# Kernel tuning notes

Hardware: AMD Instinct MI355X
Metric: run time of the kernel (lower is better)

The kernel has to match this reference:

```python
import jax, jax.numpy as jnp
import numpy as np

E = 96   # embed_dim; num_heads = 96 -> head_dim = 1, scale = 1.0
P = 4    # patch size (in_features 48 = 3 * 4 * 4)
NW = 4   # n_windows (hardcoded in apply_window_msa)


def setup_inputs() -> dict:
    key = jax.random.key(0)
    ks = jax.random.split(key, 5)
    x = jax.random.normal(ks[0], (16, 3, 256, 256), dtype=jnp.float32)
    lin_w = jax.random.normal(ks[1], (E, 48), dtype=jnp.float32) * (1.0 / np.sqrt(48).astype(np.float32))
    lin_b = jnp.zeros((E,), jnp.float32)
    in_proj_w = jax.random.normal(ks[2], (3 * E, E), dtype=jnp.float32) * (1.0 / np.sqrt(E).astype(np.float32))
    in_proj_b = jnp.zeros((3 * E,), jnp.float32)
    out_proj_w = jax.random.normal(ks[3], (E, E), dtype=jnp.float32) * (1.0 / np.sqrt(E).astype(np.float32))
    out_proj_b = jnp.zeros((E,), jnp.float32)
    return dict(x=x, lin_w=lin_w, lin_b=lin_b, in_proj_w=in_proj_w,
                in_proj_b=in_proj_b, out_proj_w=out_proj_w, out_proj_b=out_proj_b)


def reference(x, lin_w, lin_b, in_proj_w, in_proj_b, out_proj_w, out_proj_b):
    N, C, H, W = x.shape
    Hp, Wp = H // P, W // P
    # patch_merging: torch unfold(2,P,P).unfold(3,P,P) -> [N,C,Hp,Wp,P,P] -> reshape
    patches = x.reshape(N, C, Hp, P, Wp, P).transpose(0, 1, 2, 4, 3, 5)
    patches = patches.reshape(N, C * P * P, Hp, Wp)  # [N, 48, Hp, Wp]
    # apply_linear_on_axis(axis=1): acts as a 1x1 projection 48 -> E
    emb = jnp.einsum('nchw,ec->nehw', patches, lin_w) + lin_b[None, :, None, None]
    # apply_window_msa: raw reshape [N,E,Hp,Wp] -> [N, 4, L, E] (memory-order, faithful to source)
    wh, ww = Hp // 2, Wp // 2
    L = wh * ww
    xw = emb.reshape(N, NW, L, E).transpose(1, 0, 2, 3)  # [4, N, L, E]
    # torch MHA with batch_first=False: seq dim = N (samples), batch dim = L
    qkv = jnp.einsum('wnle,fe->wnlf', xw, in_proj_w) + in_proj_b  # [4, N, L, 3E]
    q, k, v = jnp.split(qkv, 3, axis=-1)  # each [4, N, L, E]; E heads of dim 1
    # head_dim = 1 -> scale = 1.0; scores over the N (sample) axis
    scores = jnp.einsum('wslh,wtlh->wlhst', q, k)        # [4, L, 96, N, N]
    attn = jax.nn.softmax(scores, axis=-1)
    out = jnp.einsum('wlhst,wtlh->wslh', attn, v)        # [4, N, L, E]
    out = jnp.einsum('wnle,fe->wnlf', out, out_proj_w) + out_proj_b
    hidden = out.transpose(1, 0, 2, 3).reshape(N, E, Hp, Wp)  # raw reshape, faithful
    return hidden
```

## Files before the change

### kernel.cpp

```cpp
#include <hip/hip_runtime.h>

#define EMB_STRIDE 393216

typedef __attribute__((ext_vector_type(8))) short short8;
typedef __attribute__((ext_vector_type(4))) float f32x4;
typedef __attribute__((ext_vector_type(2))) __fp16 f16x2;

#define MFMA16 __builtin_amdgcn_mfma_f32_16x16x32_bf16
#define SCHED_PIN() __builtin_amdgcn_sched_barrier(0)

static __device__ __forceinline__ short bf16h(float v) {
    unsigned u = __builtin_bit_cast(unsigned, v);
    unsigned r = (u + 0x7FFFu + ((u >> 16) & 1u)) >> 16;
    return (short)r;
}
static __device__ __forceinline__ float bf16f(short s) {
    unsigned u = ((unsigned)(unsigned short)s) << 16;
    return __builtin_bit_cast(float, u);
}
static __device__ __forceinline__ unsigned packsplit(float v) {
    const short h = bf16h(v);
    const float d = v - bf16f(h);
    const unsigned lo = __builtin_bit_cast(unsigned, d) >> 16;
    return ((unsigned)(unsigned short)h << 16) | lo;
}

__global__ __launch_bounds__(256) void k_prep(
    const float* __restrict__ lin_w, const float* __restrict__ in_w,
    const float* __restrict__ out_w,
    short* __restrict__ WH, short* __restrict__ WL2,
    short* __restrict__ WOH, short* __restrict__ WOL,
    short* __restrict__ WPH, short* __restrict__ WPL) {
    const int i0 = blockIdx.x * 256 + threadIdx.x;
    const int stride = gridDim.x * 256;
    for (int i = i0; i < 27648; i += stride) {
        int j = i & 7, g = (i >> 3) & 3, rest = i >> 5;
        int f = rest % 288, kc = rest / 288;
        float v = in_w[f * 96 + kc * 32 + g * 8 + j];
        short h = bf16h(v);
        WH[i] = h; WL2[i] = bf16h(v - bf16f(h));
    }
    for (int i = i0; i < 9216; i += stride) {
        int j = i & 7, g = (i >> 3) & 3, rest = i >> 5;
        int f = rest % 96, kc = rest / 96;
        float v = out_w[f * 96 + kc * 32 + g * 8 + j];
        short h = bf16h(v);
        WOH[i] = h; WOL[i] = bf16h(v - bf16f(h));
    }
    for (int i = i0; i < 6144; i += stride) {
        int j = i & 7, lane = (i >> 3) & 63, rest = i >> 9;
        int et = rest % 6, kc = rest / 6;
        int e = et * 16 + (lane & 15);
        int k = kc * 32 + (lane >> 4) * 8 + j;
        float v = (k < 48) ? lin_w[e * 48 + k] : 0.f;
        short h = bf16h(v);
        WPH[i] = h; WPL[i] = bf16h(v - bf16f(h));
    }
}

__global__ __launch_bounds__(256, 3) void k_patch(
    const float* __restrict__ x, const short* __restrict__ WPH,
    const short* __restrict__ WPL, const float* __restrict__ lin_b,
    unsigned* __restrict__ embp) {
    const int tid = threadIdx.x, wave = tid >> 6, lane = tid & 63;
    const int n = blockIdx.x >> 6;
    const int T = (blockIdx.x & 63) * 4 + wave;
    const int a = T >> 6, b = (T >> 2) & 15, cc = T & 3;
    const int col16 = lane & 15, grp = lane >> 4;
    const int d = col16 >> 2, g = col16 & 3;

    const int rowoff = (a * 4 + d) * 256 + b * 16 + cc * 4 + g;
    const int gA = (grp >> 1) * 65536 + (grp & 1) * 32768;
    const float* p0 = x + (size_t)n * 196608 + rowoff + gA;

    float v0[8], v1[8];
#pragma unroll
    for (int j = 0; j < 8; ++j) v0[j] = p0[j * 4096];
    if (grp < 2) {
#pragma unroll
        for (int j = 0; j < 8; ++j) v1[j] = p0[131072 - (grp >> 1) * 65536 + j * 4096];
    }
    SCHED_PIN();
    short8 Bh[2], Bl[2];
#pragma unroll
    for (int j = 0; j < 8; ++j) {
        const short h = bf16h(v0[j]);
        Bh[0][j] = h; Bl[0][j] = bf16h(v0[j] - bf16f(h));
        Bh[1][j] = 0; Bl[1][j] = 0;
    }
    if (grp < 2) {
#pragma unroll
        for (int j = 0; j < 8; ++j) {
            const short h = bf16h(v1[j]);
            Bh[1][j] = h; Bl[1][j] = bf16h(v1[j] - bf16f(h));
        }
    }

    f32x4 acc[6];
#pragma unroll
    for (int et = 0; et < 6; ++et) acc[et] = (f32x4){0.f, 0.f, 0.f, 0.f};
#pragma unroll
    for (int kc = 0; kc < 2; ++kc) {
        short8 AH[6], AL[6];
#pragma unroll
        for (int et = 0; et < 6; ++et)
            AH[et] = *(const short8*)(WPH + (kc * 6 + et) * 512 + lane * 8);
#pragma unroll
        for (int et = 0; et < 6; ++et)
            AL[et] = *(const short8*)(WPL + (kc * 6 + et) * 512 + lane * 8);
        SCHED_PIN();
#pragma unroll
        for (int et = 0; et < 6; ++et) acc[et] = MFMA16(AH[et], Bh[kc], acc[et], 0, 0, 0);
#pragma unroll
        for (int et = 0; et < 6; ++et) acc[et] = MFMA16(AH[et], Bl[kc], acc[et], 0, 0, 0);
#pragma unroll
        for (int et = 0; et < 6; ++et) acc[et] = MFMA16(AL[et], Bh[kc], acc[et], 0, 0, 0);
    }

    unsigned* ebase = embp + (size_t)n * EMB_STRIDE + T * 16 + col16;
#pragma unroll
    for (int et = 0; et < 6; ++et) {
        const float4 bv = *(const float4*)(lin_b + et * 16 + grp * 4);
        const float vr[4] = {acc[et][0] + bv.x, acc[et][1] + bv.y,
                             acc[et][2] + bv.z, acc[et][3] + bv.w};
#pragma unroll
        for (int r = 0; r < 4; ++r)
            ebase[(size_t)(et * 16 + grp * 4 + r) * 4096] = packsplit(vr[r]);
    }
}

__global__ __launch_bounds__(128, 3) void k_msa(
    const unsigned* __restrict__ embp,
    const short* __restrict__ WH, const short* __restrict__ WL2,
    const short* __restrict__ WOH, const short* __restrict__ WOL,
    const float* __restrict__ in_b, const float* __restrict__ out_b,
    float* __restrict__ out) {

    __shared__ unsigned AO[2][96 * 17];

    const int tid = threadIdx.x;
    const int half = tid >> 6, lane = tid & 63;
    const int wl0 = blockIdx.x * 2;
    const int n = lane & 15, g = lane >> 4;
    const int hoff = half * 1536;

    uint4 ub[12];
#pragma unroll
    for (int w = 0; w < 2; ++w) {
        const unsigned* xrow = embp + (size_t)n * EMB_STRIDE + (wl0 + w) * 96;
#pragma unroll
        for (int kc = 0; kc < 3; ++kc) {
            ub[(w * 3 + kc) * 2]     = *(const uint4*)(xrow + kc * 32 + g * 8);
            ub[(w * 3 + kc) * 2 + 1] = *(const uint4*)(xrow + kc * 32 + g * 8 + 4);
        }
    }
    SCHED_PIN();
    short8 Bh[2][3], Bl[2][3];
#pragma unroll
    for (int w = 0; w < 2; ++w)
#pragma unroll
        for (int kc = 0; kc < 3; ++kc) {
            const uint4 ua0 = ub[(w * 3 + kc) * 2], ua1 = ub[(w * 3 + kc) * 2 + 1];
            const unsigned ua[8] = {ua0.x, ua0.y, ua0.z, ua0.w, ua1.x, ua1.y, ua1.z, ua1.w};
#pragma unroll
            for (int j = 0; j < 8; ++j) {
                Bh[w][kc][j] = (short)(ua[j] >> 16);
                Bl[w][kc][j] = (short)(ua[j] & 0xffffu);
            }
        }

    f32x4 acc0[9], acc1[9];
#pragma unroll
    for (int a = 0; a < 9; ++a) {
        acc0[a] = (f32x4){0.f, 0.f, 0.f, 0.f};
        acc1[a] = (f32x4){0.f, 0.f, 0.f, 0.f};
    }
#pragma unroll
    for (int kc = 0; kc < 3; ++kc) {
        const short* whp = WH  + kc * 9216 + n * 32 + g * 8 + hoff;
        const short* wlp = WL2 + kc * 9216 + n * 32 + g * 8 + hoff;
#pragma unroll
        for (int t3 = 0; t3 < 3; ++t3) {
            short8 AH[3], AL[3];
#pragma unroll
            for (int i = 0; i < 3; ++i)
                AH[i] = *(const short8*)(whp + (t3 * 6 + i) * 512);
#pragma unroll
            for (int i = 0; i < 3; ++i)
                AL[i] = *(const short8*)(wlp + (t3 * 6 + i) * 512);
            SCHED_PIN();
#pragma unroll
            for (int i = 0; i < 3; ++i) {
                const int a = t3 * 3 + i;
                acc0[a] = MFMA16(AH[i], Bh[0][kc], acc0[a], 0, 0, 0);
                acc1[a] = MFMA16(AH[i], Bh[1][kc], acc1[a], 0, 0, 0);
                acc0[a] = MFMA16(AH[i], Bl[0][kc], acc0[a], 0, 0, 0);
                acc1[a] = MFMA16(AH[i], Bl[1][kc], acc1[a], 0, 0, 0);
                acc0[a] = MFMA16(AL[i], Bh[0][kc], acc0[a], 0, 0, 0);
                acc1[a] = MFMA16(AL[i], Bh[1][kc], acc1[a], 0, 0, 0);
            }
        }
    }
#pragma unroll
    for (int a = 0; a < 9; ++a) {
        const float4 bv = *(const float4*)(in_b + ((a / 3) * 6 + (a % 3)) * 16 + half * 48 + g * 4);
        acc0[a][0] += bv.x; acc0[a][1] += bv.y; acc0[a][2] += bv.z; acc0[a][3] += bv.w;
        acc1[a][0] += bv.x; acc1[a][1] += bv.y; acc1[a][2] += bv.z; acc1[a][3] += bv.w;
    }

    const int gbase = lane & 48;
#define ATT_BODY(ACC, W)                                                       \
    {                                                                          \
        const float q2 = ACC[c][r2] * 1.44269504f;                             \
        const f16x2 pk = __builtin_amdgcn_cvt_pkrtz(ACC[3 + c][r2], ACC[6 + c][r2]); \
        const int pki = __builtin_bit_cast(int, pk);                           \
        int kvr[16];                                                           \
        _Pragma("unroll")                                                      \
        for (int tt = 0; tt < 16; ++tt) kvr[tt] = __shfl(pki, gbase | tt, 64); \
        SCHED_PIN();                                                           \
        float sp[4] = {0.f, 0.f, 0.f, 0.f}, op[4] = {0.f, 0.f, 0.f, 0.f};      \
        _Pragma("unroll")                                                      \
        for (int tt = 0; tt < 16; ++tt) {                                      \
            const f16x2 kv2 = __builtin_bit_cast(f16x2, kvr[tt]);              \
            const float e = __builtin_amdgcn_exp2f(q2 * (float)kv2[0]);        \
            sp[tt & 3] += e;                                                   \
            op[tt & 3] = fmaf(e, (float)kv2[1], op[tt & 3]);                   \
        }                                                                      \
        const float s = (sp[0] + sp[1]) + (sp[2] + sp[3]);                     \
        const float o = (op[0] + op[1]) + (op[2] + op[3]);                     \
        AO[W][(half * 48 + c * 16 + g * 4 + r2) * 17 + n] =                    \
            packsplit(o * __builtin_amdgcn_rcpf(s));                           \
    }
#pragma unroll
    for (int c = 0; c < 3; ++c)
#pragma unroll
        for (int r2 = 0; r2 < 4; ++r2) {
            ATT_BODY(acc0, 0)
            ATT_BODY(acc1, 1)
        }
    __syncthreads();

    f32x4 oc0[3], oc1[3];
#pragma unroll
    for (int c2 = 0; c2 < 3; ++c2) {
        oc0[c2] = (f32x4){0.f, 0.f, 0.f, 0.f};
        oc1[c2] = (f32x4){0.f, 0.f, 0.f, 0.f};
    }
#pragma unroll
    for (int kc = 0; kc < 3; ++kc) {
        const short* whp = WOH + kc * 3072 + n * 32 + g * 8 + hoff;
        const short* wlp = WOL + kc * 3072 + n * 32 + g * 8 + hoff;
        short8 OAH[3], OAL[3];
#pragma unroll
        for (int c2 = 0; c2 < 3; ++c2) OAH[c2] = *(const short8*)(whp + c2 * 512);
#pragma unroll
        for (int c2 = 0; c2 < 3; ++c2) OAL[c2] = *(const short8*)(wlp + c2 * 512);
        unsigned u0[8], u1[8];
#pragma unroll
        for (int j = 0; j < 8; ++j) {
            u0[j] = AO[0][(kc * 32 + g * 8 + j) * 17 + n];
            u1[j] = AO[1][(kc * 32 + g * 8 + j) * 17 + n];
        }
        SCHED_PIN();
        short8 bh0, bl0, bh1, bl1;
#pragma unroll
        for (int j = 0; j < 8; ++j) {
            bh0[j] = (short)(u0[j] >> 16); bl0[j] = (short)(u0[j] & 0xffffu);
            bh1[j] = (short)(u1[j] >> 16); bl1[j] = (short)(u1[j] & 0xffffu);
        }
#pragma unroll
        for (int c2 = 0; c2 < 3; ++c2) oc0[c2] = MFMA16(OAH[c2], bh0, oc0[c2], 0, 0, 0);
#pragma unroll
        for (int c2 = 0; c2 < 3; ++c2) oc1[c2] = MFMA16(OAH[c2], bh1, oc1[c2], 0, 0, 0);
#pragma unroll
        for (int c2 = 0; c2 < 3; ++c2) oc0[c2] = MFMA16(OAH[c2], bl0, oc0[c2], 0, 0, 0);
#pragma unroll
        for (int c2 = 0; c2 < 3; ++c2) oc1[c2] = MFMA16(OAH[c2], bl1, oc1[c2], 0, 0, 0);
#pragma unroll
        for (int c2 = 0; c2 < 3; ++c2) oc0[c2] = MFMA16(OAL[c2], bh0, oc0[c2], 0, 0, 0);
#pragma unroll
        for (int c2 = 0; c2 < 3; ++c2) oc1[c2] = MFMA16(OAL[c2], bh1, oc1[c2], 0, 0, 0);
    }

#pragma unroll
    for (int c2 = 0; c2 < 3; ++c2) {
        const int fb = half * 48 + c2 * 16 + g * 4;
        const float4 ob = *(const float4*)(out_b + fb);
        const float4 vs0 = make_float4(oc0[c2][0] + ob.x, oc0[c2][1] + ob.y,
                                       oc0[c2][2] + ob.z, oc0[c2][3] + ob.w);
        const float4 vs1 = make_float4(oc1[c2][0] + ob.x, oc1[c2][1] + ob.y,
                                       oc1[c2][2] + ob.z, oc1[c2][3] + ob.w);
        *(float4*)(out + (size_t)n * EMB_STRIDE + wl0 * 96 + fb) = vs0;
        *(float4*)(out + (size_t)n * EMB_STRIDE + (wl0 + 1) * 96 + fb) = vs1;
    }
}

extern "C" void kernel_launch(void* const* d_in, const int* in_sizes, int n_in,
                              void* d_out, int out_size, void* d_ws, size_t ws_size,
                              hipStream_t stream) {
    const float* x     = (const float*)d_in[0];
    const float* lin_w = (const float*)d_in[1];
    const float* lin_b = (const float*)d_in[2];
    const float* in_w  = (const float*)d_in[3];
    const float* in_b  = (const float*)d_in[4];
    const float* out_w = (const float*)d_in[5];
    const float* out_b = (const float*)d_in[6];
    float* outp = (float*)d_out;

    unsigned* embp = (unsigned*)d_ws;
    short* WH  = (short*)((char*)d_ws + 25165824);
    short* WL2 = WH + 32768;
    short* WOH = WH + 65536;
    short* WOL = WH + 81920;
    short* WPH = WH + 98304;
    short* WPL = WH + 106496;

    k_prep<<<64, 256, 0, stream>>>(lin_w, in_w, out_w, WH, WL2, WOH, WOL, WPH, WPL);
    k_patch<<<1024, 256, 0, stream>>>(x, WPH, WPL, lin_b, embp);
    k_msa<<<2048, 128, 0, stream>>>(embp, WH, WL2, WOH, WOL, in_b, out_b, outp);
}
```

Before: 73.76 us.

## Split MSA work across six waves per block with shared-memory staging

The MSA kernel goes from 2 waves to 6 waves per block, so each wave owns 16 heads instead of 48. The input rows are staged once into shared memory rather than loaded by each wave, and K/V pairs are exchanged through shared memory instead of cross-lane shuffles. The aim is more parallelism and lower register pressure per wave, at the cost of extra LDS traffic and a block-wide barrier after the staging load.

```diff
diff --git a/kernel.cpp b/kernel.cpp
--- a/kernel.cpp
+++ b/kernel.cpp
@@ -129,137 +129,136 @@
     }
 }
 
-__global__ __launch_bounds__(128, 3) void k_msa(
+__global__ __launch_bounds__(384, 4) void k_msa(
     const unsigned* __restrict__ embp,
     const short* __restrict__ WH, const short* __restrict__ WL2,
     const short* __restrict__ WOH, const short* __restrict__ WOL,
     const float* __restrict__ in_b, const float* __restrict__ out_b,
     float* __restrict__ out) {
 
-    __shared__ unsigned AO[2][96 * 17];
+    __shared__ unsigned Xs[2 * 16 * 100];
+    __shared__ unsigned KV[2 * 96 * 20];
 
     const int tid = threadIdx.x;
-    const int half = tid >> 6, lane = tid & 63;
+    const int ht = tid >> 6, lane = tid & 63;
     const int wl0 = blockIdx.x * 2;
     const int n = lane & 15, g = lane >> 4;
-    const int hoff = half * 1536;
-
-    uint4 ub[12];
-#pragma unroll
-    for (int w = 0; w < 2; ++w) {
-        const unsigned* xrow = embp + (size_t)n * EMB_STRIDE + (wl0 + w) * 96;
-#pragma unroll
-        for (int kc = 0; kc < 3; ++kc) {
-            ub[(w * 3 + kc) * 2]     = *(const uint4*)(xrow + kc * 32 + g * 8);
-            ub[(w * 3 + kc) * 2 + 1] = *(const uint4*)(xrow + kc * 32 + g * 8 + 4);
-        }
-    }
-    SCHED_PIN();
-    short8 Bh[2][3], Bl[2][3];
-#pragma unroll
-    for (int w = 0; w < 2; ++w)
-#pragma unroll
-        for (int kc = 0; kc < 3; ++kc) {
-            const uint4 ua0 = ub[(w * 3 + kc) * 2], ua1 = ub[(w * 3 + kc) * 2 + 1];
-            const unsigned ua[8] = {ua0.x, ua0.y, ua0.z, ua0.w, ua1.x, ua1.y, ua1.z, ua1.w};
+
+    {
+        const int pos = tid * 4;
+        const int sn = pos / 96, se = pos % 96;
+#pragma unroll
+        for (int w = 0; w < 2; ++w) {
+            const uint4 v = *(const uint4*)(embp + (size_t)sn * EMB_STRIDE + (wl0 + w) * 96 + se);
+            *(uint4*)(&Xs[w * 1600 + sn * 100 + se]) = v;
+        }
+    }
+    __syncthreads();
+
+    f32x4 acc0[3], acc1[3];
+#pragma unroll
+    for (int i = 0; i < 3; ++i) {
+        acc0[i] = (f32x4){0.f, 0.f, 0.f, 0.f};
+        acc1[i] = (f32x4){0.f, 0.f, 0.f, 0.f};
+    }
+#pragma unroll
+    for (int kc = 0; kc < 3; ++kc) {
+        const uint4 xa0 = *(const uint4*)(&Xs[n * 100 + kc * 32 + g * 8]);
+        const uint4 xa1 = *(const uint4*)(&Xs[n * 100 + kc * 32 + g * 8 + 4]);
+        const uint4 xb0 = *(const uint4*)(&Xs[1600 + n * 100 + kc * 32 + g * 8]);
+        const uint4 xb1 = *(const uint4*)(&Xs[1600 + n * 100 + kc * 32 + g * 8 + 4]);
+        const short* whp = WH  + kc * 9216 + ht * 512 + n * 32 + g * 8;
+        const short* wlp = WL2 + kc * 9216 + ht * 512 + n * 32 + g * 8;
+        short8 AH[3], AL[3];
+#pragma unroll
+        for (int i = 0; i < 3; ++i) AH[i] = *(const short8*)(whp + i * 3072);
+#pragma unroll
+        for (int i = 0; i < 3; ++i) AL[i] = *(const short8*)(wlp + i * 3072);
+        SCHED_PIN();
+        short8 Bh0, Bl0, Bh1, Bl1;
+        {
+            const unsigned ua[8] = {xa0.x, xa0.y, xa0.z, xa0.w, xa1.x, xa1.y, xa1.z, xa1.w};
+            const unsigned ub[8] = {xb0.x, xb0.y, xb0.z, xb0.w, xb1.x, xb1.y, xb1.z, xb1.w};
 #pragma unroll
             for (int j = 0; j < 8; ++j) {
-                Bh[w][kc][j] = (short)(ua[j] >> 16);
-                Bl[w][kc][j] = (short)(ua[j] & 0xffffu);
+                Bh0[j] = (short)(ua[j] >> 16); Bl0[j] = (short)(ua[j] & 0xffffu);
+                Bh1[j] = (short)(ub[j] >> 16); Bl1[j] = (short)(ub[j] & 0xffffu);
             }
         }
-
-    f32x4 acc0[9], acc1[9];
-#pragma unroll
-    for (int a = 0; a < 9; ++a) {
-        acc0[a] = (f32x4){0.f, 0.f, 0.f, 0.f};
-        acc1[a] = (f32x4){0.f, 0.f, 0.f, 0.f};
-    }
-#pragma unroll
-    for (int kc = 0; kc < 3; ++kc) {
-        const short* whp = WH  + kc * 9216 + n * 32 + g * 8 + hoff;
-        const short* wlp = WL2 + kc * 9216 + n * 32 + g * 8 + hoff;
-#pragma unroll
-        for (int t3 = 0; t3 < 3; ++t3) {
-            short8 AH[3], AL[3];
-#pragma unroll
-            for (int i = 0; i < 3; ++i)
-                AH[i] = *(const short8*)(whp + (t3 * 6 + i) * 512);
-#pragma unroll
-            for (int i = 0; i < 3; ++i)
-                AL[i] = *(const short8*)(wlp + (t3 * 6 + i) * 512);
-            SCHED_PIN();
-#pragma unroll
-            for (int i = 0; i < 3; ++i) {
-                const int a = t3 * 3 + i;
-                acc0[a] = MFMA16(AH[i], Bh[0][kc], acc0[a], 0, 0, 0);
-                acc1[a] = MFMA16(AH[i], Bh[1][kc], acc1[a], 0, 0, 0);
-                acc0[a] = MFMA16(AH[i], Bl[0][kc], acc0[a], 0, 0, 0);
-                acc1[a] = MFMA16(AH[i], Bl[1][kc], acc1[a], 0, 0, 0);
-                acc0[a] = MFMA16(AL[i], Bh[0][kc], acc0[a], 0, 0, 0);
-                acc1[a] = MFMA16(AL[i], Bh[1][kc], acc1[a], 0, 0, 0);
-            }
-        }
-    }
-#pragma unroll
-    for (int a = 0; a < 9; ++a) {
-        const float4 bv = *(const float4*)(in_b + ((a / 3) * 6 + (a % 3)) * 16 + half * 48 + g * 4);
-        acc0[a][0] += bv.x; acc0[a][1] += bv.y; acc0[a][2] += bv.z; acc0[a][3] += bv.w;
-        acc1[a][0] += bv.x; acc1[a][1] += bv.y; acc1[a][2] += bv.z; acc1[a][3] += bv.w;
-    }
-
-    const int gbase = lane & 48;
-#define ATT_BODY(ACC, W)                                                       \
+#pragma unroll
+        for (int i = 0; i < 3; ++i) acc0[i] = MFMA16(AH[i], Bh0, acc0[i], 0, 0, 0);
+#pragma unroll
+        for (int i = 0; i < 3; ++i) acc1[i] = MFMA16(AH[i], Bh1, acc1[i], 0, 0, 0);
+#pragma unroll
+        for (int i = 0; i < 3; ++i) acc0[i] = MFMA16(AH[i], Bl0, acc0[i], 0, 0, 0);
+#pragma unroll
+        for (int i = 0; i < 3; ++i) acc1[i] = MFMA16(AH[i], Bl1, acc1[i], 0, 0, 0);
+#pragma unroll
+        for (int i = 0; i < 3; ++i) acc0[i] = MFMA16(AL[i], Bh0, acc0[i], 0, 0, 0);
+#pragma unroll
+        for (int i = 0; i < 3; ++i) acc1[i] = MFMA16(AL[i], Bh1, acc1[i], 0, 0, 0);
+    }
+#pragma unroll
+    for (int i = 0; i < 3; ++i) {
+        const float4 bv = *(const float4*)(in_b + i * 96 + ht * 16 + g * 4);
+        acc0[i][0] += bv.x; acc0[i][1] += bv.y; acc0[i][2] += bv.z; acc0[i][3] += bv.w;
+        acc1[i][0] += bv.x; acc1[i][1] += bv.y; acc1[i][2] += bv.z; acc1[i][3] += bv.w;
+    }
+
+#pragma unroll
+    for (int r2 = 0; r2 < 4; ++r2) {
+        const int h = ht * 16 + g * 4 + r2;
+        const f16x2 p0 = __builtin_amdgcn_cvt_pkrtz(acc0[1][r2], acc0[2][r2]);
+        const f16x2 p1 = __builtin_amdgcn_cvt_pkrtz(acc1[1][r2], acc1[2][r2]);
+        KV[h * 20 + n] = __builtin_bit_cast(unsigned, p0);
+        KV[1920 + h * 20 + n] = __builtin_bit_cast(unsigned, p1);
+    }
+
+    unsigned ao0[4], ao1[4];
+#define ATT_BODY(ACC, WOFF, AOARR)                                             \
     {                                                                          \
-        const float q2 = ACC[c][r2] * 1.44269504f;                             \
-        const f16x2 pk = __builtin_amdgcn_cvt_pkrtz(ACC[3 + c][r2], ACC[6 + c][r2]); \
-        const int pki = __builtin_bit_cast(int, pk);                           \
-        int kvr[16];                                                           \
-        _Pragma("unroll")                                                      \
-        for (int tt = 0; tt < 16; ++tt) kvr[tt] = __shfl(pki, gbase | tt, 64); \
-        SCHED_PIN();                                                           \
+        const float q2 = ACC[0][r2] * 1.44269504f;                             \
+        const uint4* row = (const uint4*)(&KV[WOFF + (ht * 16 + g * 4 + r2) * 20]); \
+        const uint4 ra = row[0], rb = row[1], rc = row[2], rd = row[3];        \
+        const unsigned kv[16] = {ra.x, ra.y, ra.z, ra.w, rb.x, rb.y, rb.z, rb.w, \
+                                 rc.x, rc.y, rc.z, rc.w, rd.x, rd.y, rd.z, rd.w}; \
         float sp[4] = {0.f, 0.f, 0.f, 0.f}, op[4] = {0.f, 0.f, 0.f, 0.f};      \
         _Pragma("unroll")                                                      \
         for (int tt = 0; tt < 16; ++tt) {                                      \
-            const f16x2 kv2 = __builtin_bit_cast(f16x2, kvr[tt]);              \
+            const f16x2 kv2 = __builtin_bit_cast(f16x2, kv[tt]);               \
             const float e = __builtin_amdgcn_exp2f(q2 * (float)kv2[0]);        \
             sp[tt & 3] += e;                                                   \
             op[tt & 3] = fmaf(e, (float)kv2[1], op[tt & 3]);                   \
         }                                                                      \
         const float s = (sp[0] + sp[1]) + (sp[2] + sp[3]);                     \
         const float o = (op[0] + op[1]) + (op[2] + op[3]);                     \
-        AO[W][(half * 48 + c * 16 + g * 4 + r2) * 17 + n] =                    \
-            packsplit(o * __builtin_amdgcn_rcpf(s));                           \
-    }
-#pragma unroll
-    for (int c = 0; c < 3; ++c)
-#pragma unroll
-        for (int r2 = 0; r2 < 4; ++r2) {
-            ATT_BODY(acc0, 0)
-            ATT_BODY(acc1, 1)
-        }
+        AOARR[r2] = packsplit(o * __builtin_amdgcn_rcpf(s));                   \
+    }
+#pragma unroll
+    for (int r2 = 0; r2 < 4; ++r2) {
+        ATT_BODY(acc0, 0, ao0)
+        ATT_BODY(acc1, 1920, ao1)
+    }
+
+#pragma unroll
+    for (int r2 = 0; r2 < 4; ++r2) {
+        const int h = ht * 16 + g * 4 + r2;
+        KV[h * 20 + n] = ao0[r2];
+        KV[1920 + h * 20 + n] = ao1[r2];
+    }
     __syncthreads();
 
-    f32x4 oc0[3], oc1[3];
-#pragma unroll
-    for (int c2 = 0; c2 < 3; ++c2) {
-        oc0[c2] = (f32x4){0.f, 0.f, 0.f, 0.f};
-        oc1[c2] = (f32x4){0.f, 0.f, 0.f, 0.f};
-    }
+    f32x4 oc0 = (f32x4){0.f, 0.f, 0.f, 0.f};
+    f32x4 oc1 = (f32x4){0.f, 0.f, 0.f, 0.f};
 #pragma unroll
     for (int kc = 0; kc < 3; ++kc) {
-        const short* whp = WOH + kc * 3072 + n * 32 + g * 8 + hoff;
-        const short* wlp = WOL + kc * 3072 + n * 32 + g * 8 + hoff;
-        short8 OAH[3], OAL[3];
-#pragma unroll
-        for (int c2 = 0; c2 < 3; ++c2) OAH[c2] = *(const short8*)(whp + c2 * 512);
-#pragma unroll
-        for (int c2 = 0; c2 < 3; ++c2) OAL[c2] = *(const short8*)(wlp + c2 * 512);
+        const short8 OAH = *(const short8*)(WOH + kc * 3072 + ht * 512 + n * 32 + g * 8);
+        const short8 OAL = *(const short8*)(WOL + kc * 3072 + ht * 512 + n * 32 + g * 8);
         unsigned u0[8], u1[8];
 #pragma unroll
         for (int j = 0; j < 8; ++j) {
-            u0[j] = AO[0][(kc * 32 + g * 8 + j) * 17 + n];
-            u1[j] = AO[1][(kc * 32 + g * 8 + j) * 17 + n];
+            u0[j] = KV[(kc * 32 + g * 8 + j) * 20 + n];
+            u1[j] = KV[1920 + (kc * 32 + g * 8 + j) * 20 + n];
         }
         SCHED_PIN();
         short8 bh0, bl0, bh1, bl1;
@@ -268,28 +267,21 @@
             bh0[j] = (short)(u0[j] >> 16); bl0[j] = (short)(u0[j] & 0xffffu);
             bh1[j] = (short)(u1[j] >> 16); bl1[j] = (short)(u1[j] & 0xffffu);
         }
-#pragma unroll
-        for (int c2 = 0; c2 < 3; ++c2) oc0[c2] = MFMA16(OAH[c2], bh0, oc0[c2], 0, 0, 0);
-#pragma unroll
-        for (int c2 = 0; c2 < 3; ++c2) oc1[c2] = MFMA16(OAH[c2], bh1, oc1[c2], 0, 0, 0);
-#pragma unroll
-        for (int c2 = 0; c2 < 3; ++c2) oc0[c2] = MFMA16(OAH[c2], bl0, oc0[c2], 0, 0, 0);
-#pragma unroll
-        for (int c2 = 0; c2 < 3; ++c2) oc1[c2] = MFMA16(OAH[c2], bl1, oc1[c2], 0, 0, 0);
-#pragma unroll
-        for (int c2 = 0; c2 < 3; ++c2) oc0[c2] = MFMA16(OAL[c2], bh0, oc0[c2], 0, 0, 0);
-#pragma unroll
-        for (int c2 = 0; c2 < 3; ++c2) oc1[c2] = MFMA16(OAL[c2], bh1, oc1[c2], 0, 0, 0);
-    }
-
-#pragma unroll
-    for (int c2 = 0; c2 < 3; ++c2) {
-        const int fb = half * 48 + c2 * 16 + g * 4;
+        oc0 = MFMA16(OAH, bh0, oc0, 0, 0, 0);
+        oc1 = MFMA16(OAH, bh1, oc1, 0, 0, 0);
+        oc0 = MFMA16(OAH, bl0, oc0, 0, 0, 0);
+        oc1 = MFMA16(OAH, bl1, oc1, 0, 0, 0);
+        oc0 = MFMA16(OAL, bh0, oc0, 0, 0, 0);
+        oc1 = MFMA16(OAL, bh1, oc1, 0, 0, 0);
+    }
+
+    {
+        const int fb = ht * 16 + g * 4;
         const float4 ob = *(const float4*)(out_b + fb);
-        const float4 vs0 = make_float4(oc0[c2][0] + ob.x, oc0[c2][1] + ob.y,
-                                       oc0[c2][2] + ob.z, oc0[c2][3] + ob.w);
-        const float4 vs1 = make_float4(oc1[c2][0] + ob.x, oc1[c2][1] + ob.y,
-                                       oc1[c2][2] + ob.z, oc1[c2][3] + ob.w);
+        const float4 vs0 = make_float4(oc0[0] + ob.x, oc0[1] + ob.y,
+                                       oc0[2] + ob.z, oc0[3] + ob.w);
+        const float4 vs1 = make_float4(oc1[0] + ob.x, oc1[1] + ob.y,
+                                       oc1[2] + ob.z, oc1[3] + ob.w);
         *(float4*)(out + (size_t)n * EMB_STRIDE + wl0 * 96 + fb) = vs0;
         *(float4*)(out + (size_t)n * EMB_STRIDE + (wl0 + 1) * 96 + fb) = vs1;
     }
@@ -317,5 +309,5 @@
 
     k_prep<<<64, 256, 0, stream>>>(lin_w, in_w, out_w, WH, WL2, WOH, WOL, WPH, WPL);
     k_patch<<<1024, 256, 0, stream>>>(x, WPH, WPL, lin_b, embp);
-    k_msa<<<2048, 128, 0, stream>>>(embp, WH, WL2, WOH, WOL, in_b, out_b, outp);
-}
+    k_msa<<<2048, 384, 0, stream>>>(embp, WH, WL2, WOH, WOL, in_b, out_b, outp);
+}
```

Result: faster. 67.41 us (-8.6%).
